# Performance work log

Hardware: AMD Instinct MI355X
Metric: run time of the kernel (lower is better)

The kernel has to match this reference:

```python
import jax, jax.numpy as jnp
import numpy as np

HIDDEN = 4096
K = 4          # Gibbs sampling steps
LR = 0.01
IMG = (16, 64, 64, 3)  # batch, H, W, C


def setup_inputs() -> dict:
    key = jax.random.key(0)
    k1, k2 = jax.random.split(key)
    inputs = jax.random.uniform(k1, IMG, dtype=jnp.float32)
    flat = IMG[1] * IMG[2] * IMG[3]
    # GlorotNormal init: std = sqrt(2 / (fan_in + fan_out))
    scale = (2.0 / (flat + HIDDEN)) ** 0.5
    W = jax.random.normal(k2, (flat, HIDDEN), dtype=jnp.float32) * scale
    a = jnp.zeros((flat, 1), dtype=jnp.float32)
    b = jnp.zeros((HIDDEN, 1), dtype=jnp.float32)
    return {"inputs": inputs, "W": W, "a": a, "b": b}


def reference(inputs, W, a, b):
    B = inputs.shape[0]
    flat = inputs.shape[1] * inputs.shape[2] * inputs.shape[3]
    vs = inputs.reshape(B, flat, 1)  # each sample is a (flat,1) column vector

    def per_sample(carry, v):
        W, a, b = carry
        v_init = v
        # k Gibbs steps: h = sigma(b + W^T v); v = sigma(a + W h)
        h = None
        for _ in range(K):
            h = jax.nn.sigmoid(b + W.T @ v)
            v = jax.nn.sigmoid(a + W @ h)
        h_init = jax.nn.sigmoid(b + W.T @ v_init)
        # Contrastive divergence with .assign (replace, not accumulate) as in source
        W_new = LR * (v_init @ h_init.T - v @ h.T)
        a_new = LR * (v_init - v)
        b_new = LR * (h_init - h)
        return (W_new, a_new, b_new), v

    _, vs_out = jax.lax.scan(per_sample, (W, a, b), vs)
    # call() returns self.v, i.e. the reconstruction of the LAST batch element
    return vs_out[-1]
```

## Files before the change

### kernel.cpp

```cpp
#include <hip/hip_runtime.h>
#include <math.h>

#define FLAT 12288
#define NH   4096
#define KSTEPS 4
#define LRC 0.01f
#define NSEG 384
#define RPS  32
#define WSCALE 64.0f
#define WINV   0.015625f

typedef float v2f __attribute__((ext_vector_type(2)));

__device__ __forceinline__ float sigm(float x) {
    return __builtin_amdgcn_rcpf(1.0f + __expf(-x));
}

template <int CTRL>
__device__ __forceinline__ float dpp_add(float x) {
    int s = __builtin_amdgcn_update_dpp(0, __float_as_int(x), CTRL, 0xf, 0xf, true);
    return x + __int_as_float(s);
}
__device__ __forceinline__ float wave_sum63(float x) {
    x = dpp_add<0x111>(x);
    x = dpp_add<0x112>(x);
    x = dpp_add<0x114>(x);
    x = dpp_add<0x118>(x);
    x = dpp_add<0x142>(x);
    x = dpp_add<0x143>(x);
    return x;
}


__global__ __launch_bounds__(256) void k_colpart_cvt(const float* __restrict__ W,
                                                     const float* __restrict__ v,
                                                     float* __restrict__ partials,
                                                     unsigned int* __restrict__ W8) {
    const float4* W4 = (const float4*)W;
    int c4 = blockIdx.x * 256 + threadIdx.x;
    int r0 = blockIdx.y * RPS;
    float4 acc = make_float4(0.f, 0.f, 0.f, 0.f);
    for (int r = r0; r < r0 + RPS; ++r) {
        float vr = v[r];
        float4 w = W4[(size_t)r * (NH / 4) + c4];
        acc.x = fmaf(w.x, vr, acc.x);
        acc.y = fmaf(w.y, vr, acc.y);
        acc.z = fmaf(w.z, vr, acc.z);
        acc.w = fmaf(w.w, vr, acc.w);
        unsigned int p = 0;
        p = __builtin_amdgcn_cvt_pk_fp8_f32(w.x * WSCALE, w.y * WSCALE, p, false);
        p = __builtin_amdgcn_cvt_pk_fp8_f32(w.z * WSCALE, w.w * WSCALE, p, true);
        W8[(size_t)r * (NH / 4) + c4] = p;
    }
    ((float4*)partials)[(size_t)blockIdx.y * (NH / 4) + c4] = acc;
}

__global__ __launch_bounds__(256) void k_colpart_fp8(const uint4* __restrict__ W8,
                                                     const float* __restrict__ v,
                                                     float* __restrict__ partials) {
    int c16 = threadIdx.x;
    int r0 = blockIdx.x * RPS;
    float acc[16];
#pragma unroll
    for (int i = 0; i < 16; i++) acc[i] = 0.f;
    for (int r = r0; r < r0 + RPS; ++r) {
        float vr = v[r] * WINV;
        uint4 w = W8[(size_t)r * (NH / 16) + c16];
        v2f f;
        f = __builtin_amdgcn_cvt_pk_f32_fp8(w.x, false); acc[0]  = fmaf(f.x, vr, acc[0]);  acc[1]  = fmaf(f.y, vr, acc[1]);
        f = __builtin_amdgcn_cvt_pk_f32_fp8(w.x, true);  acc[2]  = fmaf(f.x, vr, acc[2]);  acc[3]  = fmaf(f.y, vr, acc[3]);
        f = __builtin_amdgcn_cvt_pk_f32_fp8(w.y, false); acc[4]  = fmaf(f.x, vr, acc[4]);  acc[5]  = fmaf(f.y, vr, acc[5]);
        f = __builtin_amdgcn_cvt_pk_f32_fp8(w.y, true);  acc[6]  = fmaf(f.x, vr, acc[6]);  acc[7]  = fmaf(f.y, vr, acc[7]);
        f = __builtin_amdgcn_cvt_pk_f32_fp8(w.z, false); acc[8]  = fmaf(f.x, vr, acc[8]);  acc[9]  = fmaf(f.y, vr, acc[9]);
        f = __builtin_amdgcn_cvt_pk_f32_fp8(w.z, true);  acc[10] = fmaf(f.x, vr, acc[10]); acc[11] = fmaf(f.y, vr, acc[11]);
        f = __builtin_amdgcn_cvt_pk_f32_fp8(w.w, false); acc[12] = fmaf(f.x, vr, acc[12]); acc[13] = fmaf(f.y, vr, acc[13]);
        f = __builtin_amdgcn_cvt_pk_f32_fp8(w.w, true);  acc[14] = fmaf(f.x, vr, acc[14]); acc[15] = fmaf(f.y, vr, acc[15]);
    }
    float4* P = (float4*)(partials + (size_t)blockIdx.x * NH + (size_t)c16 * 16);
#pragma unroll
    for (int q = 0; q < 4; q++) {
        float4 o; o.x = acc[4*q]; o.y = acc[4*q+1]; o.z = acc[4*q+2]; o.w = acc[4*q+3];
        P[q] = o;
    }
}

__global__ __launch_bounds__(256) void k_hreduce(const float* __restrict__ partials,
                                                 const float* __restrict__ b,
                                                 float* __restrict__ h,
                                                 float* __restrict__ hi) {
    int c  = threadIdx.x & 31;
    int sg = threadIdx.x >> 5;
    int col = blockIdx.x * 32 + c;
    float s = 0.f;
    for (int g = sg; g < NSEG; g += 8) s += partials[(size_t)g * NH + col];
    __shared__ float red[8][33];
    red[sg][c] = s;
    __syncthreads();
    if (threadIdx.x < 32) {
        float t = 0.f;
#pragma unroll
        for (int g2 = 0; g2 < 8; g2++) t += red[g2][threadIdx.x];
        float hh = sigm(t + b[col]);
        h[col] = hh;
        if (hi) hi[col] = hh;
    }
}

__global__ __launch_bounds__(256) void k_vstep_fp8(const unsigned char* __restrict__ W8,
                                                   const float* __restrict__ h,
                                                   const float* __restrict__ a,
                                                   float* __restrict__ v) {
    int wid = threadIdx.x >> 6, lane = threadIdx.x & 63;
    int row = blockIdx.x * 4 + wid;
    const uint4* Wr = (const uint4*)(W8 + (size_t)row * NH);
    const float4* h4 = (const float4*)h;
    float acc = 0.f;
    for (int k = lane; k < NH / 16; k += 64) {
        uint4 w = Wr[k];
        float4 h0 = h4[4*k], h1 = h4[4*k+1], h2 = h4[4*k+2], h3 = h4[4*k+3];
        v2f f;
        f = __builtin_amdgcn_cvt_pk_f32_fp8(w.x, false); acc = fmaf(f.x, h0.x, acc); acc = fmaf(f.y, h0.y, acc);
        f = __builtin_amdgcn_cvt_pk_f32_fp8(w.x, true);  acc = fmaf(f.x, h0.z, acc); acc = fmaf(f.y, h0.w, acc);
        f = __builtin_amdgcn_cvt_pk_f32_fp8(w.y, false); acc = fmaf(f.x, h1.x, acc); acc = fmaf(f.y, h1.y, acc);
        f = __builtin_amdgcn_cvt_pk_f32_fp8(w.y, true);  acc = fmaf(f.x, h1.z, acc); acc = fmaf(f.y, h1.w, acc);
        f = __builtin_amdgcn_cvt_pk_f32_fp8(w.z, false); acc = fmaf(f.x, h2.x, acc); acc = fmaf(f.y, h2.y, acc);
        f = __builtin_amdgcn_cvt_pk_f32_fp8(w.z, true);  acc = fmaf(f.x, h2.z, acc); acc = fmaf(f.y, h2.w, acc);
        f = __builtin_amdgcn_cvt_pk_f32_fp8(w.w, false); acc = fmaf(f.x, h3.x, acc); acc = fmaf(f.y, h3.y, acc);
        f = __builtin_amdgcn_cvt_pk_f32_fp8(w.w, true);  acc = fmaf(f.x, h3.z, acc); acc = fmaf(f.y, h3.w, acc);
    }
    acc = wave_sum63(acc);
    if (lane == 63) v[row] = sigm(a[row] + acc * WINV);
}


#define TB  512
#define RVB (FLAT / TB)
#define RHB (NH / TB)
#define NWAVES (TB / 64)

__global__ __launch_bounds__(512) void k_phaseB(const float* __restrict__ inputs,
                                                const float* __restrict__ hi0,
                                                const float* __restrict__ hk0,
                                                const float* __restrict__ vk0,
                                                float* __restrict__ out) {
    int t = threadIdx.x;
    int lane = t & 63, wid = t >> 6;
    __shared__ float2 red[2][NWAVES];

    float Vi[RVB], Vk[RVB], v[RVB];
    float Hi[RHB], Hk[RHB], h[RHB], hini[RHB];

#pragma unroll
    for (int r = 0; r < RVB; r++) { int i = r * TB + t; Vi[r] = inputs[i]; Vk[r] = vk0[i]; }
#pragma unroll
    for (int r = 0; r < RHB; r++) { int j = r * TB + t; Hi[r] = hi0[j]; Hk[r] = hk0[j]; }

    int rc = 0;
    for (int s = 1; s < 16; ++s) {
        const float* vin = inputs + (size_t)s * FLAT;
#pragma unroll
        for (int r = 0; r < RVB; r++) v[r] = vin[r * TB + t];

        for (int k = 0; k < KSTEPS; ++k) {
            float px0 = 0.f, px1 = 0.f, py0 = 0.f, py1 = 0.f;
#pragma unroll
            for (int r = 0; r < RVB; r += 2) {
                px0 = fmaf(Vi[r],   v[r],   px0); py0 = fmaf(Vk[r],   v[r],   py0);
                px1 = fmaf(Vi[r+1], v[r+1], px1); py1 = fmaf(Vk[r+1], v[r+1], py1);
            }
            float px = wave_sum63(px0 + px1), py = wave_sum63(py0 + py1);
            if (lane == 63) { float2 w2; w2.x = px; w2.y = py; red[rc & 1][wid] = w2; }
            __syncthreads();
            float al = 0.f, be = 0.f;
#pragma unroll
            for (int w = 0; w < NWAVES; w++) { float2 w2 = red[rc & 1][w]; al += w2.x; be += w2.y; }
            rc++;
            float ca = LRC * (1.f + al), cb = LRC * (1.f + be);

            float qx = 0.f, qy = 0.f;
#pragma unroll
            for (int r = 0; r < RHB; r++) {
                float hh = sigm(ca * Hi[r] - cb * Hk[r]);
                h[r] = hh;
                if (k == 0) hini[r] = hh;
                qx = fmaf(Hi[r], hh, qx); qy = fmaf(Hk[r], hh, qy);
            }
            qx = wave_sum63(qx); qy = wave_sum63(qy);
            if (lane == 63) { float2 w2; w2.x = qx; w2.y = qy; red[rc & 1][wid] = w2; }
            __syncthreads();
            float ga = 0.f, de = 0.f;
#pragma unroll
            for (int w = 0; w < NWAVES; w++) { float2 w2 = red[rc & 1][w]; ga += w2.x; de += w2.y; }
            rc++;
            float cg = LRC * (1.f + ga), cd = LRC * (1.f + de);

#pragma unroll
            for (int r = 0; r < RVB; r++) v[r] = sigm(cg * Vi[r] - cd * Vk[r]);
        }

#pragma unroll
        for (int r = 0; r < RVB; r++) { Vk[r] = v[r]; Vi[r] = vin[r * TB + t]; }
#pragma unroll
        for (int r = 0; r < RHB; r++) { Hk[r] = h[r]; Hi[r] = hini[r]; }
    }

#pragma unroll
    for (int r = 0; r < RVB; r++) out[r * TB + t] = Vk[r];
}


extern "C" void kernel_launch(void* const* d_in, const int* in_sizes, int n_in,
                              void* d_out, int out_size, void* d_ws, size_t ws_size,
                              hipStream_t stream) {
    const float* inputs = (const float*)d_in[0];
    const float* W      = (const float*)d_in[1];
    const float* a_in   = (const float*)d_in[2];
    const float* b_in   = (const float*)d_in[3];
    float* out = (float*)d_out;

    unsigned int* W8 = (unsigned int*)d_ws;
    float* partials = (float*)((char*)d_ws + (size_t)FLAT * NH);
    float* h  = partials + (size_t)NSEG * NH;
    float* hi = h + NH;
    float* v  = hi + NH;

    dim3 blk(256);

    k_colpart_cvt<<<dim3(4, NSEG), blk, 0, stream>>>(W, inputs, partials, W8);
    k_hreduce<<<dim3(NH / 32), blk, 0, stream>>>(partials, b_in, h, hi);
    k_vstep_fp8<<<dim3(FLAT / 4), blk, 0, stream>>>((const unsigned char*)W8, h, a_in, v);

    for (int k = 1; k < KSTEPS; ++k) {
        k_colpart_fp8<<<dim3(NSEG), blk, 0, stream>>>((const uint4*)W8, v, partials);
        k_hreduce<<<dim3(NH / 32), blk, 0, stream>>>(partials, b_in, h, (float*)nullptr);
        k_vstep_fp8<<<dim3(FLAT / 4), blk, 0, stream>>>((const unsigned char*)W8, h, a_in, v);
    }

    k_phaseB<<<1, TB, 0, stream>>>(inputs, hi, h, v, out);
}
```

Before: 537.7 us.

## Fuse visible-step and hidden partial products into one pass over FP8 weights

Replaces the separate v-step and column-partial kernels in Gibbs steps 2..K with a fused kernel. Each wave loads a W row once, computes v[r] via dot with h, then reuses the same row to accumulate hidden partial sums. This removes one full read of the FP8 weight matrix per iteration, at the cost of twice as many partial segments to reduce, fewer blocks, and heavy register use with low occupancy.

```diff
diff --git a/kernel.cpp b/kernel.cpp
--- a/kernel.cpp
+++ b/kernel.cpp
@@ -7,6 +7,7 @@
 #define LRC 0.01f
 #define NSEG 384
 #define RPS  32
+#define NSEG2 768
 #define WSCALE 64.0f
 #define WINV   0.015625f
 
@@ -55,44 +56,16 @@
     ((float4*)partials)[(size_t)blockIdx.y * (NH / 4) + c4] = acc;
 }
 
-__global__ __launch_bounds__(256) void k_colpart_fp8(const uint4* __restrict__ W8,
-                                                     const float* __restrict__ v,
-                                                     float* __restrict__ partials) {
-    int c16 = threadIdx.x;
-    int r0 = blockIdx.x * RPS;
-    float acc[16];
-#pragma unroll
-    for (int i = 0; i < 16; i++) acc[i] = 0.f;
-    for (int r = r0; r < r0 + RPS; ++r) {
-        float vr = v[r] * WINV;
-        uint4 w = W8[(size_t)r * (NH / 16) + c16];
-        v2f f;
-        f = __builtin_amdgcn_cvt_pk_f32_fp8(w.x, false); acc[0]  = fmaf(f.x, vr, acc[0]);  acc[1]  = fmaf(f.y, vr, acc[1]);
-        f = __builtin_amdgcn_cvt_pk_f32_fp8(w.x, true);  acc[2]  = fmaf(f.x, vr, acc[2]);  acc[3]  = fmaf(f.y, vr, acc[3]);
-        f = __builtin_amdgcn_cvt_pk_f32_fp8(w.y, false); acc[4]  = fmaf(f.x, vr, acc[4]);  acc[5]  = fmaf(f.y, vr, acc[5]);
-        f = __builtin_amdgcn_cvt_pk_f32_fp8(w.y, true);  acc[6]  = fmaf(f.x, vr, acc[6]);  acc[7]  = fmaf(f.y, vr, acc[7]);
-        f = __builtin_amdgcn_cvt_pk_f32_fp8(w.z, false); acc[8]  = fmaf(f.x, vr, acc[8]);  acc[9]  = fmaf(f.y, vr, acc[9]);
-        f = __builtin_amdgcn_cvt_pk_f32_fp8(w.z, true);  acc[10] = fmaf(f.x, vr, acc[10]); acc[11] = fmaf(f.y, vr, acc[11]);
-        f = __builtin_amdgcn_cvt_pk_f32_fp8(w.w, false); acc[12] = fmaf(f.x, vr, acc[12]); acc[13] = fmaf(f.y, vr, acc[13]);
-        f = __builtin_amdgcn_cvt_pk_f32_fp8(w.w, true);  acc[14] = fmaf(f.x, vr, acc[14]); acc[15] = fmaf(f.y, vr, acc[15]);
-    }
-    float4* P = (float4*)(partials + (size_t)blockIdx.x * NH + (size_t)c16 * 16);
-#pragma unroll
-    for (int q = 0; q < 4; q++) {
-        float4 o; o.x = acc[4*q]; o.y = acc[4*q+1]; o.z = acc[4*q+2]; o.w = acc[4*q+3];
-        P[q] = o;
-    }
-}
-
 __global__ __launch_bounds__(256) void k_hreduce(const float* __restrict__ partials,
                                                  const float* __restrict__ b,
                                                  float* __restrict__ h,
-                                                 float* __restrict__ hi) {
+                                                 float* __restrict__ hi,
+                                                 int nseg) {
     int c  = threadIdx.x & 31;
     int sg = threadIdx.x >> 5;
     int col = blockIdx.x * 32 + c;
     float s = 0.f;
-    for (int g = sg; g < NSEG; g += 8) s += partials[(size_t)g * NH + col];
+    for (int g = sg; g < nseg; g += 8) s += partials[(size_t)g * NH + col];
     __shared__ float red[8][33];
     red[sg][c] = s;
     __syncthreads();
@@ -103,6 +76,81 @@
         float hh = sigm(t + b[col]);
         h[col] = hh;
         if (hi) hi[col] = hh;
+    }
+}
+
+__global__ __launch_bounds__(256, 1) void k_fused(const unsigned char* __restrict__ W8,
+                                                  const float* __restrict__ h,
+                                                  const float* __restrict__ a,
+                                                  float* __restrict__ v,
+                                                  float* __restrict__ partials) {
+    int lane = threadIdx.x & 63, wv = threadIdx.x >> 6;
+    int rbase = blockIdx.x * 64 + wv * 16;
+    const float4* h4 = (const float4*)h;
+
+    float4 hreg[16];
+#pragma unroll
+    for (int j = 0; j < 4; j++) {
+        int k = lane + 64 * j;
+#pragma unroll
+        for (int q = 0; q < 4; q++) hreg[4 * j + q] = h4[4 * k + q];
+    }
+
+    float pacc[64];
+#pragma unroll
+    for (int i = 0; i < 64; i++) pacc[i] = 0.f;
+
+    for (int i = 0; i < 16; ++i) {
+        int r = rbase + i;
+        const uint4* Wr = (const uint4*)(W8 + (size_t)r * NH);
+        uint4 wq[4];
+#pragma unroll
+        for (int j = 0; j < 4; j++) wq[j] = Wr[lane + 64 * j];
+
+        float dot = 0.f;
+#pragma unroll
+        for (int j = 0; j < 4; j++) {
+            v2f f;
+            f = __builtin_amdgcn_cvt_pk_f32_fp8(wq[j].x, false); dot = fmaf(f.x, hreg[4*j].x, dot);   dot = fmaf(f.y, hreg[4*j].y, dot);
+            f = __builtin_amdgcn_cvt_pk_f32_fp8(wq[j].x, true);  dot = fmaf(f.x, hreg[4*j].z, dot);   dot = fmaf(f.y, hreg[4*j].w, dot);
+            f = __builtin_amdgcn_cvt_pk_f32_fp8(wq[j].y, false); dot = fmaf(f.x, hreg[4*j+1].x, dot); dot = fmaf(f.y, hreg[4*j+1].y, dot);
+            f = __builtin_amdgcn_cvt_pk_f32_fp8(wq[j].y, true);  dot = fmaf(f.x, hreg[4*j+1].z, dot); dot = fmaf(f.y, hreg[4*j+1].w, dot);
+            f = __builtin_amdgcn_cvt_pk_f32_fp8(wq[j].z, false); dot = fmaf(f.x, hreg[4*j+2].x, dot); dot = fmaf(f.y, hreg[4*j+2].y, dot);
+            f = __builtin_amdgcn_cvt_pk_f32_fp8(wq[j].z, true);  dot = fmaf(f.x, hreg[4*j+2].z, dot); dot = fmaf(f.y, hreg[4*j+2].w, dot);
+            f = __builtin_amdgcn_cvt_pk_f32_fp8(wq[j].w, false); dot = fmaf(f.x, hreg[4*j+3].x, dot); dot = fmaf(f.y, hreg[4*j+3].y, dot);
+            f = __builtin_amdgcn_cvt_pk_f32_fp8(wq[j].w, true);  dot = fmaf(f.x, hreg[4*j+3].z, dot); dot = fmaf(f.y, hreg[4*j+3].w, dot);
+        }
+        dot = wave_sum63(dot);
+        float full = __shfl(dot, 63);
+        float vr = sigm(a[r] + full * WINV);
+        if (lane == 63) v[r] = vr;
+
+        float vs = vr * WINV;
+#pragma unroll
+        for (int j = 0; j < 4; j++) {
+            v2f f;
+            f = __builtin_amdgcn_cvt_pk_f32_fp8(wq[j].x, false); pacc[16*j+0]  = fmaf(f.x, vs, pacc[16*j+0]);  pacc[16*j+1]  = fmaf(f.y, vs, pacc[16*j+1]);
+            f = __builtin_amdgcn_cvt_pk_f32_fp8(wq[j].x, true);  pacc[16*j+2]  = fmaf(f.x, vs, pacc[16*j+2]);  pacc[16*j+3]  = fmaf(f.y, vs, pacc[16*j+3]);
+            f = __builtin_amdgcn_cvt_pk_f32_fp8(wq[j].y, false); pacc[16*j+4]  = fmaf(f.x, vs, pacc[16*j+4]);  pacc[16*j+5]  = fmaf(f.y, vs, pacc[16*j+5]);
+            f = __builtin_amdgcn_cvt_pk_f32_fp8(wq[j].y, true);  pacc[16*j+6]  = fmaf(f.x, vs, pacc[16*j+6]);  pacc[16*j+7]  = fmaf(f.y, vs, pacc[16*j+7]);
+            f = __builtin_amdgcn_cvt_pk_f32_fp8(wq[j].z, false); pacc[16*j+8]  = fmaf(f.x, vs, pacc[16*j+8]);  pacc[16*j+9]  = fmaf(f.y, vs, pacc[16*j+9]);
+            f = __builtin_amdgcn_cvt_pk_f32_fp8(wq[j].z, true);  pacc[16*j+10] = fmaf(f.x, vs, pacc[16*j+10]); pacc[16*j+11] = fmaf(f.y, vs, pacc[16*j+11]);
+            f = __builtin_amdgcn_cvt_pk_f32_fp8(wq[j].w, false); pacc[16*j+12] = fmaf(f.x, vs, pacc[16*j+12]); pacc[16*j+13] = fmaf(f.y, vs, pacc[16*j+13]);
+            f = __builtin_amdgcn_cvt_pk_f32_fp8(wq[j].w, true);  pacc[16*j+14] = fmaf(f.x, vs, pacc[16*j+14]); pacc[16*j+15] = fmaf(f.y, vs, pacc[16*j+15]);
+        }
+    }
+
+    float* P = partials + (size_t)(blockIdx.x * 4 + wv) * NH;
+#pragma unroll
+    for (int j = 0; j < 4; j++) {
+        float4* Pj = (float4*)(P + 16 * (lane + 64 * j));
+#pragma unroll
+        for (int q = 0; q < 4; q++) {
+            float4 o;
+            o.x = pacc[16*j + 4*q + 0]; o.y = pacc[16*j + 4*q + 1];
+            o.z = pacc[16*j + 4*q + 2]; o.w = pacc[16*j + 4*q + 3];
+            Pj[q] = o;
+        }
     }
 }
 
@@ -220,21 +268,20 @@
 
     unsigned int* W8 = (unsigned int*)d_ws;
     float* partials = (float*)((char*)d_ws + (size_t)FLAT * NH);
-    float* h  = partials + (size_t)NSEG * NH;
+    float* h  = partials + (size_t)NSEG2 * NH;
     float* hi = h + NH;
     float* v  = hi + NH;
 
     dim3 blk(256);
 
     k_colpart_cvt<<<dim3(4, NSEG), blk, 0, stream>>>(W, inputs, partials, W8);
-    k_hreduce<<<dim3(NH / 32), blk, 0, stream>>>(partials, b_in, h, hi);
+    k_hreduce<<<dim3(NH / 32), blk, 0, stream>>>(partials, b_in, h, hi, NSEG);
+
+    for (int k = 1; k < KSTEPS; ++k) {
+        k_fused<<<dim3(FLAT / 64), blk, 0, stream>>>((const unsigned char*)W8, h, a_in, v, partials);
+        k_hreduce<<<dim3(NH / 32), blk, 0, stream>>>(partials, b_in, h, (float*)nullptr, NSEG2);
+    }
     k_vstep_fp8<<<dim3(FLAT / 4), blk, 0, stream>>>((const unsigned char*)W8, h, a_in, v);
 
-    for (int k = 1; k < KSTEPS; ++k) {
-        k_colpart_fp8<<<dim3(NSEG), blk, 0, stream>>>((const uint4*)W8, v, partials);
-        k_hreduce<<<dim3(NH / 32), blk, 0, stream>>>(partials, b_in, h, (float*)nullptr);
-        k_vstep_fp8<<<dim3(FLAT / 4), blk, 0, stream>>>((const unsigned char*)W8, h, a_in, v);
-    }
-
     k_phaseB<<<1, TB, 0, stream>>>(inputs, hi, h, v, out);
 }
```

New measurement: 546.5 us. No clear change (+1.7%).
